# Performance work log

Measured on AMD Instinct MI355X. Metric: run time of the kernel, lower is better.

Reference implementation:

```python
import jax, jax.numpy as jnp
import numpy as np
from jax import lax

B, T, Tq, S, G, Hd, GW, V = 128, 512, 32, 64, 300, 256, 512, 159
Z = 7 * Hd + 2


def _gru_cell(x, h, Wih, Whh, bih, bhh):
    # torch.nn.GRUCell math (gate order r,z,n)
    gi = x @ Wih.T + bih
    gh = h @ Whh.T + bhh
    i_r, i_z, i_n = jnp.split(gi, 3, axis=-1)
    h_r, h_z, h_n = jnp.split(gh, 3, axis=-1)
    r = jax.nn.sigmoid(i_r + h_r)
    z = jax.nn.sigmoid(i_z + h_z)
    n = jnp.tanh(i_n + r * h_n)
    return (1.0 - z) * n + z * h


def _run_gru(x, Wih, Whh, bih, bhh):
    b = x.shape[0]
    h0 = jnp.zeros((b, Whh.shape[1]), x.dtype)
    def step(h, xt):
        h2 = _gru_cell(xt, h, Wih, Whh, bih, bhh)
        return h2, h2
    _, ys = lax.scan(step, h0, jnp.swapaxes(x, 0, 1))
    return jnp.swapaxes(ys, 0, 1)  # [B,T,H]


def _attention(C, Qv, Mv, zW, gW1, gb1, gW2, gb2):
    # Attention(C, Q, Mt_1) -> Attention_G(c, m=Q, q=Mt_1); vectorized over sentences.
    qb = Qv[:, None, :]   # question, 2nd arg 'm' in Attention_Z
    mb = Mv[:, None, :]   # memory,   3rd arg 'q' in Attention_Z
    cW = jnp.einsum('bsh,kh->bsk', C, zW)  # att_zW(c), no bias
    z = jnp.concatenate([
        C,
        jnp.broadcast_to(qb, C.shape),
        jnp.broadcast_to(mb, C.shape),
        C * mb,                       # c * q  (q = memory)
        C * qb,                       # c * m  (m = question)
        jnp.abs(C - mb),              # |c - q|
        jnp.abs(C - qb),              # |c - m|
        jnp.sum(cW * mb, -1, keepdims=True),  # diag(cW q^T)
        jnp.sum(cW * qb, -1, keepdims=True),  # diag(cW m^T)
    ], axis=-1)  # [B,S,7H+2]
    H1 = jnp.tanh(jnp.einsum('bsz,gz->bsg', z, gW1) + gb1)
    g = jax.nn.sigmoid(jnp.einsum('bsg,og->bso', H1, gW2) + gb2)
    return g[..., 0]  # [B,S]


def setup_inputs() -> dict:
    key = jax.random.key(0)
    ks = jax.random.split(key, 32)
    def p(k, shape):
        return jax.random.normal(k, shape, jnp.float32) * 0.05
    inp = {
        'input': jax.random.normal(ks[0], (B, T, G), jnp.float32),
        'Q': jax.random.normal(ks[1], (B, Tq, G), jnp.float32),
        'EOS_idx': jnp.sort(jax.random.randint(ks[2], (B, S), 0, T), axis=1),
        'q_seq_len': jax.random.randint(ks[3], (B,), 0, Tq),
        'm_depth': 3,
        'a_len': 1,
        # GRU_i
        'Wih_i': p(ks[4], (3 * Hd, G)), 'Whh_i': p(ks[5], (3 * Hd, Hd)),
        'bih_i': p(ks[6], (3 * Hd,)), 'bhh_i': p(ks[7], (3 * Hd,)),
        # GRU_q
        'Wih_q': p(ks[8], (3 * Hd, G)), 'Whh_q': p(ks[9], (3 * Hd, Hd)),
        'bih_q': p(ks[10], (3 * Hd,)), 'bhh_q': p(ks[11], (3 * Hd,)),
        # attention
        'zW': p(ks[12], (Hd, Hd)),
        'gW1': p(ks[13], (GW, Z)), 'gb1': p(ks[14], (GW,)),
        'gW2': p(ks[15], (1, GW)), 'gb2': p(ks[16], (1,)),
        # GRUcell_m
        'Wih_m': p(ks[17], (3 * Hd, Hd)), 'Whh_m': p(ks[18], (3 * Hd, Hd)),
        'bih_m': p(ks[19], (3 * Hd,)), 'bhh_m': p(ks[20], (3 * Hd,)),
        # answer module
        'Wa': p(ks[21], (V, Hd)),
        'Wih_a': p(ks[22], (3 * Hd, Hd + V)), 'Whh_a': p(ks[23], (3 * Hd, Hd)),
        'bih_a': p(ks[24], (3 * Hd,)), 'bhh_a': p(ks[25], (3 * Hd,)),
    }
    return inp


def reference(input, Q, EOS_idx, q_seq_len, m_depth, a_len,
              Wih_i, Whh_i, bih_i, bhh_i,
              Wih_q, Whh_q, bih_q, bhh_q,
              zW, gW1, gb1, gW2, gb2,
              Wih_m, Whh_m, bih_m, bhh_m,
              Wa, Wih_a, Whh_a, bih_a, bhh_a):
    b = input.shape[0]
    # InputModule2: GRU over words, gather hidden states at EOS positions -> facts
    out_i = _run_gru(input, Wih_i, Whh_i, bih_i, bhh_i)          # [B,T,H]
    facts = out_i[jnp.arange(b)[:, None], EOS_idx]               # [B,S,H]
    # QuestionModule2: last valid hidden state of question GRU
    out_q = _run_gru(Q, Wih_q, Whh_q, bih_q, bhh_q)              # [B,Tq,H]
    qidx = jnp.clip(q_seq_len - 1, 0, Q.shape[1] - 1)
    q = out_q[jnp.arange(b), qidx]                               # [B,H]
    # MemoryUpdate (mode='softmax')
    Mt = q
    atts = []
    for _ in range(m_depth):
        att = _attention(facts, q, Mt, zW, gW1, gb1, gW2, gb2)   # [B,S]
        atts.append(att[:, None, :])
        soft = jax.nn.softmax(att, axis=1)
        Htc = jnp.einsum('bsh,bs->bh', facts, soft)              # SoftmaxRep
        Mt = _gru_cell(Htc, Mt, Wih_m, Whh_m, bih_m, bhh_m)
    Attentions = jnp.concatenate(atts, axis=1)                   # [B,depth,S]
    # AnswerModule
    at = Mt
    yt = jax.nn.softmax(at @ Wa.T, axis=1)
    preds = []
    for _ in range(a_len):
        xt = jnp.concatenate([yt, q], axis=1)
        at = _gru_cell(xt, at, Wih_a, Whh_a, bih_a, bhh_a)
        yt = jax.nn.softmax(at @ Wa.T, axis=1)
        preds.append(yt)
    pred = jnp.concatenate(preds, axis=1)                        # [B, a_len*159]
    return pred
```

## Files before the change

kernel.cpp:

```cpp
#include <hip/hip_runtime.h>
#include <hip/hip_bf16.h>

#define B_   128
#define T_   512
#define TQ_  32
#define S_   64
#define G_   300
#define GP_  320
#define HD_  256
#define GW_  512
#define V_   159
#define Z_   1794
#define ZP_  1824
#define H3_  768

using bf16x8 = __attribute__((ext_vector_type(8))) short;
using bf16x4 = __attribute__((ext_vector_type(4))) short;
using f32x4  = __attribute__((ext_vector_type(4))) float;

#define OFF_WIHB_I 0u
#define OFF_WIHB_Q 491520u
#define OFF_GW1B   983040u
#define OFF_FACTS  2850816u
#define OFF_QVEC   11239424u
#define OFF_UQ     11370496u
#define OFF_UM     11501568u
#define OFF_MT     11632640u
#define OFF_B2I    13139968u
#define OFF_B2Q    13143040u
#define OFF_QBF    13500416u
#define OFF_ABF    16777216u
#define OFF_GIQ    20971520u
#define OFF_Z      29360128u
#define OFF_WMXT   59768832u
#define OFF_WMHT   60555264u
#define OFF_WAXT   61341696u
#define OFF_WAHT   62616576u
#define OFF_GII    67108864u
#define OFF_H1     67108864u

#define WAIT_LGKM0() __builtin_amdgcn_s_waitcnt(0xC07F)

__device__ __forceinline__ unsigned short f2bf(float f) {
    unsigned int u = __float_as_uint(f);
    u += 0x7fffu + ((u >> 16) & 1u);
    return (unsigned short)(u >> 16);
}
__device__ __forceinline__ float bf2f(unsigned short s) {
    return __uint_as_float(((unsigned int)s) << 16);
}
__device__ __forceinline__ float rcpf(float x) { return __builtin_amdgcn_rcpf(x); }
__device__ __forceinline__ float sigm(float x) { return rcpf(1.f + __expf(-x)); }
__device__ __forceinline__ float tanh_fast(float x) {
    float e = __expf(-2.f * fabsf(x));
    float t = (1.f - e) * rcpf(1.f + e);
    return copysignf(t, x);
}

#define S1_ 196608
#define S2_ 318720
#define S3_ 768
#define S4_ 245760
#define S5_ 933888
#define S6_ 1310720
#define S7_ 20971520
#define PREP_TOT (S1_ + S2_ + S3_ + S4_ + S5_ + S6_ + S7_)
__global__ void prep_kernel(
    const float* __restrict__ Wih_m, float* __restrict__ WmxT,
    const float* __restrict__ Whh_m, float* __restrict__ WmhT,
    const float* __restrict__ Wih_a, float* __restrict__ WaxT,
    const float* __restrict__ Whh_a, float* __restrict__ WahT,
    const float* __restrict__ bih_i, const float* __restrict__ bhh_i, float* __restrict__ b2i,
    const float* __restrict__ bih_q, const float* __restrict__ bhh_q, float* __restrict__ b2q,
    const float* __restrict__ Wih_i, unsigned short* __restrict__ Wihb_i,
    const float* __restrict__ Wih_q, unsigned short* __restrict__ Wihb_q,
    const float* __restrict__ gW1,   unsigned short* __restrict__ gW1b,
    const float* __restrict__ Qin,   unsigned short* __restrict__ Qbf,
    const float* __restrict__ input, unsigned short* __restrict__ Abf)
{
    int i = blockIdx.x * 256 + threadIdx.x;
    if (i < S1_) {
        int r = i / 256, k = i - r * 256;
        WmxT[(size_t)k * 768 + r] = Wih_m[i];
        WmhT[(size_t)k * 768 + r] = Whh_m[i];
        WahT[(size_t)k * 768 + r] = Whh_a[i];
        return;
    }
    i -= S1_;
    if (i < S2_) {
        int r = i / 415, k = i - r * 415;
        WaxT[(size_t)k * 768 + r] = Wih_a[i];
        return;
    }
    i -= S2_;
    if (i < S3_) {
        b2i[i] = bih_i[i] + (i < 512 ? bhh_i[i] : 0.f);
        b2q[i] = bih_q[i] + (i < 512 ? bhh_q[i] : 0.f);
        return;
    }
    i -= S3_;
    if (i < S4_) {
        int r = i / GP_, c = i - r * GP_;
        Wihb_i[i] = (c < G_) ? f2bf(Wih_i[(size_t)r * G_ + c]) : (unsigned short)0;
        Wihb_q[i] = (c < G_) ? f2bf(Wih_q[(size_t)r * G_ + c]) : (unsigned short)0;
        return;
    }
    i -= S4_;
    if (i < S5_) {
        int r = i / ZP_, c = i - r * ZP_;
        gW1b[i] = (c < Z_) ? f2bf(gW1[(size_t)r * Z_ + c]) : (unsigned short)0;
        return;
    }
    i -= S5_;
    if (i < S6_) {
        int r = i / GP_, c = i - r * GP_;
        Qbf[i] = (c < G_) ? f2bf(Qin[(size_t)r * G_ + c]) : (unsigned short)0;
        return;
    }
    i -= S6_;
    if (i < S7_) {
        int r = i / GP_, c = i - r * GP_;
        Abf[i] = (c < G_) ? f2bf(input[(size_t)r * G_ + c]) : (unsigned short)0;
    }
}

__global__ __launch_bounds__(256) void gemm_bf16_kernel(
    const unsigned short* __restrict__ A, const unsigned short* __restrict__ W,
    const float* __restrict__ bias, void* __restrict__ Cout,
    int M, int N, int Kp, int act, int out_bf16, int mode, int logT)
{
    __shared__ unsigned short As[64][40];
    __shared__ unsigned short Bs[64][40];
    int tid  = threadIdx.x;
    int wv   = tid >> 6, lane = tid & 63;
    int l15  = lane & 15, q = lane >> 4;
    int n0   = blockIdx.x * 64, m0 = blockIdx.y * 64;
    int r    = tid >> 2, p4 = tid & 3;

    const f32x4 zero4 = {0.f, 0.f, 0.f, 0.f};
    f32x4 acc[4] = {zero4, zero4, zero4, zero4};

    for (int k0 = 0; k0 < Kp; k0 += 32) {
        *(int4*)&As[r][p4 * 8] = *(const int4*)&A[(size_t)(m0 + r) * Kp + k0 + p4 * 8];
        *(int4*)&Bs[r][p4 * 8] = *(const int4*)&W[(size_t)(n0 + r) * Kp + k0 + p4 * 8];
        __syncthreads();
        bf16x8 af = *(const bf16x8*)&As[16 * wv + l15][q * 8];
#pragma unroll
        for (int nt = 0; nt < 4; nt++) {
            bf16x8 bf = *(const bf16x8*)&Bs[16 * nt + l15][q * 8];
            acc[nt] = __builtin_amdgcn_mfma_f32_16x16x32_bf16(af, bf, acc[nt], 0, 0, 0);
        }
        __syncthreads();
    }
    int rb = q * 4;
#pragma unroll
    for (int nt = 0; nt < 4; nt++) {
        int cgate = n0 + 16 * nt + l15;
        float bv = bias ? bias[cgate] : 0.f;
#pragma unroll
        for (int i = 0; i < 4; i++) {
            int row = m0 + 16 * wv + rb + i;
            float v = acc[nt][i] + bv;
            if (act == 1) v = tanh_fast(v);
            if (mode == 1) {
                int Tl = 1 << logT;
                int b = row >> logT, t = row & (Tl - 1);
                int cc = b >> 4, l = b & 15;
                int type = cgate >> 8, h = cgate & 255;
                int wvd = h >> 5, off = h & 31;
                int ttd = off >> 4, qd = (off >> 2) & 3, id = off & 3;
                int tidd = wvd * 64 + qd * 16 + l;
                size_t addr = ((size_t)(cc * Tl + t) * 512 + tidd) * 24 + type * 8 + ttd * 4 + id;
                ((unsigned short*)Cout)[addr] = f2bf(v);
            } else if (out_bf16) {
                ((unsigned short*)Cout)[(size_t)row * N + cgate] = f2bf(v);
            } else {
                ((float*)Cout)[(size_t)row * N + cgate] = v;
            }
        }
    }
}

__global__ __launch_bounds__(512, 2) void gru_rec_kernel(
    const float* __restrict__ Whh0, const float* __restrict__ bhh0,
    const unsigned short* __restrict__ gi0, int T0, const int* __restrict__ g0, int GL0,
    float* __restrict__ dst0,
    const float* __restrict__ Whh1, const float* __restrict__ bhh1,
    const unsigned short* __restrict__ gi1, int T1, const int* __restrict__ g1, int GL1,
    float* __restrict__ dst1)
{
    __shared__ unsigned short hfr[2][8][4][16][8];
    __shared__ int glist[16 * 64];
    __shared__ int gptr[16], gr0s[2][16], gr1s[2][16];
    extern __shared__ unsigned short wnL[];

    int cb  = blockIdx.x;
    int tid = threadIdx.x;
    int wv  = tid >> 6, lane = tid & 63;
    int l15 = lane & 15, q = lane >> 4;

    const float* Whh; const float* bhh; const unsigned short* gi;
    const int* gidx; float* gdst; int T, GL, isq, c;
    if (cb < 8) { Whh = Whh0; bhh = bhh0; gi = gi0; T = T0; gidx = g0; GL = GL0; isq = 0; gdst = dst0; c = cb; }
    else        { Whh = Whh1; bhh = bhh1; gi = gi1; T = T1; gidx = g1; GL = GL1; isq = 1; gdst = dst1; c = cb - 8; }

    bf16x8 wf[5][8];
#pragma unroll
    for (int mt = 0; mt < 5; mt++) {
        int type = (mt < 4) ? (mt >> 1) : 2;
        int tt   = (mt < 4) ? (mt & 1) : 0;
        int g = type * 256 + 32 * wv + 16 * tt + l15;
#pragma unroll
        for (int ks = 0; ks < 8; ks++) {
            float4 w0 = *(const float4*)&Whh[(size_t)g * 256 + ks * 32 + q * 8];
            float4 w1 = *(const float4*)&Whh[(size_t)g * 256 + ks * 32 + q * 8 + 4];
            bf16x8 v;
            v[0] = (short)f2bf(w0.x); v[1] = (short)f2bf(w0.y);
            v[2] = (short)f2bf(w0.z); v[3] = (short)f2bf(w0.w);
            v[4] = (short)f2bf(w1.x); v[5] = (short)f2bf(w1.y);
            v[6] = (short)f2bf(w1.z); v[7] = (short)f2bf(w1.w);
            wf[mt][ks] = v;
        }
    }
    {
        int g = 512 + 32 * wv + 16 + l15;
#pragma unroll
        for (int ks = 0; ks < 8; ks++) {
            float4 w0 = *(const float4*)&Whh[(size_t)g * 256 + ks * 32 + q * 8];
            float4 w1 = *(const float4*)&Whh[(size_t)g * 256 + ks * 32 + q * 8 + 4];
            bf16x8 v;
            v[0] = (short)f2bf(w0.x); v[1] = (short)f2bf(w0.y);
            v[2] = (short)f2bf(w0.z); v[3] = (short)f2bf(w0.w);
            v[4] = (short)f2bf(w1.x); v[5] = (short)f2bf(w1.y);
            v[6] = (short)f2bf(w1.z); v[7] = (short)f2bf(w1.w);
            *(bf16x8*)&wnL[((wv * 8 + ks) * 64 + lane) * 8] = v;
        }
    }
    float bn[2][4];
#pragma unroll
    for (int tt = 0; tt < 2; tt++)
#pragma unroll
        for (int i = 0; i < 4; i++)
            bn[tt][i] = bhh[512 + 32 * wv + 16 * tt + 4 * q + i];

    for (int i2 = tid; i2 < 2048; i2 += 512) ((int*)hfr)[i2] = 0;
    for (int i2 = tid; i2 < 16 * GL; i2 += 512) {
        int b = i2 / GL, s = i2 - b * GL;
        int raw = gidx[(c * 16 + b) * GL + s];
        if (isq) { raw -= 1; if (raw < 0) raw = 0; if (raw > T - 1) raw = T - 1; }
        glist[b * 64 + s] = raw;
    }
    __syncthreads();
    if (tid < 16) {
        int p = 0;
        while (p < GL && glist[tid * 64 + p] == 0) p++;
        gr0s[0][tid] = 0; gr1s[0][tid] = p; gptr[tid] = p;
    }
    __syncthreads();

    float hprev[2][4] = {{0.f, 0.f, 0.f, 0.f}, {0.f, 0.f, 0.f, 0.f}};
    const unsigned short* gib = gi + (size_t)c * T * 12288;
    bf16x8 xa, xb, xc;
    {
        const unsigned short* pv = gib + (size_t)tid * 24;
        xa = *(const bf16x8*)pv;
        xb = *(const bf16x8*)(pv + 8);
        xc = *(const bf16x8*)(pv + 16);
    }

    const f32x4 zero4 = {0.f, 0.f, 0.f, 0.f};
    for (int t = 0; t < T; t++) {
        int cur = t & 1, nxt = cur ^ 1;
        if (tid < 16) {
            int tt1 = t + 1;
            int p = gptr[tid], pp = p;
            while (p < GL && glist[tid * 64 + p] == tt1) p++;
            gr0s[nxt][tid] = pp; gr1s[nxt][tid] = p; gptr[tid] = p;
        }
        f32x4 acc[6];
        acc[0] = zero4; acc[1] = zero4; acc[2] = zero4; acc[3] = zero4;
        {
            f32x4 b4 = {bn[0][0], bn[0][1], bn[0][2], bn[0][3]}; acc[4] = b4;
            f32x4 b5 = {bn[1][0], bn[1][1], bn[1][2], bn[1][3]}; acc[5] = b5;
        }
#pragma unroll
        for (int ks = 0; ks < 8; ks++) {
            bf16x8 hb = *(const bf16x8*)&hfr[cur][ks][q][l15][0];
            acc[0] = __builtin_amdgcn_mfma_f32_16x16x32_bf16(wf[0][ks], hb, acc[0], 0, 0, 0);
            acc[1] = __builtin_amdgcn_mfma_f32_16x16x32_bf16(wf[1][ks], hb, acc[1], 0, 0, 0);
            acc[2] = __builtin_amdgcn_mfma_f32_16x16x32_bf16(wf[2][ks], hb, acc[2], 0, 0, 0);
            acc[3] = __builtin_amdgcn_mfma_f32_16x16x32_bf16(wf[3][ks], hb, acc[3], 0, 0, 0);
            acc[4] = __builtin_amdgcn_mfma_f32_16x16x32_bf16(wf[4][ks], hb, acc[4], 0, 0, 0);
            bf16x8 w5 = *(const bf16x8*)&wnL[((wv * 8 + ks) * 64 + lane) * 8];
            acc[5] = __builtin_amdgcn_mfma_f32_16x16x32_bf16(w5, hb, acc[5], 0, 0, 0);
        }
        float h2a[2][4];
#pragma unroll
        for (int tt = 0; tt < 2; tt++) {
#pragma unroll
            for (int i = 0; i < 4; i++) {
                float r = sigm(bf2f((unsigned short)xa[tt * 4 + i]) + acc[tt][i]);
                float z = sigm(bf2f((unsigned short)xb[tt * 4 + i]) + acc[2 + tt][i]);
                float n = tanh_fast(bf2f((unsigned short)xc[tt * 4 + i]) + r * acc[4 + tt][i]);
                float h2 = (1.f - z) * n + z * hprev[tt][i];
                hprev[tt][i] = h2;
                h2a[tt][i] = h2;
            }
            bf16x4 hb;
#pragma unroll
            for (int i = 0; i < 4; i++) hb[i] = (short)f2bf(h2a[tt][i]);
            int qp = 2 * tt + (q >> 1), jb = 4 * (q & 1);
            *(bf16x4*)&hfr[nxt][wv][qp][l15][jb] = hb;
        }
        {
            int p0 = gr0s[cur][l15], p1 = gr1s[cur][l15];
            for (int s = p0; s < p1; s++) {
                float* dp = &gdst[((size_t)(c * 16 + l15) * GL + s) * 256 + 32 * wv + 4 * q];
                float4 o0 = {h2a[0][0], h2a[0][1], h2a[0][2], h2a[0][3]};
                float4 o1 = {h2a[1][0], h2a[1][1], h2a[1][2], h2a[1][3]};
                *(float4*)dp        = o0;
                *(float4*)(dp + 16) = o1;
            }
        }
        {
            int tn = (t + 1 < T) ? (t + 1) : (T - 1);
            const unsigned short* pv = gib + ((size_t)tn * 512 + tid) * 24;
            xa = *(const bf16x8*)pv;
            xb = *(const bf16x8*)(pv + 8);
            xc = *(const bf16x8*)(pv + 16);
        }
        __builtin_amdgcn_sched_barrier(0);
        WAIT_LGKM0();
        __builtin_amdgcn_s_barrier();
        __builtin_amdgcn_sched_barrier(0);
    }
}

__global__ __launch_bounds__(256) void uvec_kernel(const float* __restrict__ zW,
                                                   const float* __restrict__ v,
                                                   float* __restrict__ u_q,
                                                   float* __restrict__ u_m,
                                                   float* __restrict__ Mt) {
    int b = blockIdx.x, h = threadIdx.x;
    float a = 0.f;
    for (int k = 0; k < 256; k++) a += zW[k * 256 + h] * v[b * 256 + k];
    u_q[b * 256 + h] = a;
    u_m[b * 256 + h] = a;
    Mt[b * 256 + h]  = v[b * 256 + h];
}

__global__ __launch_bounds__(256) void build_z_kernel(
    const float* __restrict__ facts, const float* __restrict__ qv, const float* __restrict__ Mt,
    const float* __restrict__ u_m, const float* __restrict__ u_q, unsigned short* __restrict__ z)
{
    __shared__ float rm[4], rq[4], szm, szq;
    int bs = blockIdx.x;
    int b  = bs >> 6;
    int j  = threadIdx.x;
    float C  = facts[(size_t)bs * 256 + j];
    float m  = Mt[b * 256 + j];
    float qq = qv[b * 256 + j];
    float dm = C * u_m[b * 256 + j];
    float dq = C * u_q[b * 256 + j];
    for (int o = 32; o; o >>= 1) { dm += __shfl_down(dm, o); dq += __shfl_down(dq, o); }
    int wvi = j >> 6;
    if ((j & 63) == 0) { rm[wvi] = dm; rq[wvi] = dq; }
    __syncthreads();
    if (j == 0) { szm = rm[0] + rm[1] + rm[2] + rm[3]; szq = rq[0] + rq[1] + rq[2] + rq[3]; }
    __syncthreads();
    size_t zr = (size_t)bs * ZP_;
    z[zr + j]        = f2bf(C);
    z[zr + 256 + j]  = f2bf(qq);
    z[zr + 512 + j]  = f2bf(m);
    z[zr + 768 + j]  = f2bf(C * m);
    z[zr + 1024 + j] = f2bf(C * qq);
    z[zr + 1280 + j] = f2bf(fabsf(C - m));
    z[zr + 1536 + j] = f2bf(fabsf(C - qq));
    if (j == 0) { z[zr + 1792] = f2bf(szm); z[zr + 1793] = f2bf(szq); }
    if (j < ZP_ - Z_) z[zr + Z_ + j] = 0;
}

__global__ __launch_bounds__(256) void episode_tail_kernel(
    const float* __restrict__ H1, const float* __restrict__ gW2, const float* __restrict__ gb2,
    const float* __restrict__ facts,
    const float* __restrict__ WmxT, const float* __restrict__ bxm,
    const float* __restrict__ WmhT, const float* __restrict__ bhm,
    const float* __restrict__ zW,
    float* __restrict__ Mt, float* __restrict__ u_m)
{
    __shared__ float red[64][4];
    __shared__ float p64[64];
    __shared__ float xs[256];
    __shared__ float hs[256];
    __shared__ float hs2[256];
    int b = blockIdx.x, tid = threadIdx.x;
    {
        int s = tid >> 2, part = tid & 3;
        const float* h1r = H1 + ((size_t)(b * 64 + s)) * 512 + part * 128;
        const float* w2  = gW2 + part * 128;
        float a = 0.f;
        for (int k = 0; k < 128; k++) a += h1r[k] * w2[k];
        red[s][part] = a;
    }
    hs[tid] = Mt[b * 256 + tid];
    __syncthreads();
    if (tid < 64) {
        float att = sigm(red[tid][0] + red[tid][1] + red[tid][2] + red[tid][3] + gb2[0]);
        float mx = att;
        for (int o = 32; o; o >>= 1) mx = fmaxf(mx, __shfl_xor(mx, o));
        float e = __expf(att - mx);
        float sm = e;
        for (int o = 32; o; o >>= 1) sm += __shfl_xor(sm, o);
        p64[tid] = e * rcpf(sm);
    }
    __syncthreads();
    {
        float a = 0.f;
        for (int s = 0; s < 64; s++) a += facts[((size_t)b * 64 + s) * 256 + tid] * p64[s];
        xs[tid] = a;
    }
    __syncthreads();
    {
        int j = tid;
        float ar = bxm[j], az = bxm[256 + j], an = bxm[512 + j];
        for (int k = 0; k < 256; k++) {
            float xv = xs[k];
            const float* wr = &WmxT[(size_t)k * 768];
            ar += xv * wr[j]; az += xv * wr[256 + j]; an += xv * wr[512 + j];
        }
        float hr = bhm[j], hz = bhm[256 + j], hn = bhm[512 + j];
        for (int k = 0; k < 256; k++) {
            float hv = hs[k];
            const float* wr = &WmhT[(size_t)k * 768];
            hr += hv * wr[j]; hz += hv * wr[256 + j]; hn += hv * wr[512 + j];
        }
        float r = sigm(ar + hr);
        float z = sigm(az + hz);
        float n = tanh_fast(an + r * hn);
        float h2 = (1.f - z) * n + z * hs[j];
        Mt[b * 256 + j] = h2;
        hs2[j] = h2;
    }
    __syncthreads();
    {
        float a = 0.f;
        for (int k = 0; k < 256; k++) a += zW[k * 256 + tid] * hs2[k];
        u_m[b * 256 + tid] = a;
    }
}

__global__ __launch_bounds__(256) void answer_kernel(
    const float* __restrict__ Mt, const float* __restrict__ Wa, const float* __restrict__ qv,
    const float* __restrict__ WaxT, const float* __restrict__ bxa,
    const float* __restrict__ WahT, const float* __restrict__ bha,
    float* __restrict__ out)
{
    __shared__ float sc[V_];
    __shared__ float xs[416];
    __shared__ float hs[256], hs2[256];
    int b = blockIdx.x, tid = threadIdx.x;
    hs[tid] = Mt[b * 256 + tid];
    xs[V_ + tid] = qv[b * 256 + tid];
    __syncthreads();
    if (tid < V_) {
        float a = 0.f;
        for (int k = 0; k < 256; k++) a += hs[k] * Wa[(size_t)tid * 256 + k];
        sc[tid] = a;
    }
    __syncthreads();
    if (tid == 0) {
        float mx = -1e30f;
        for (int v = 0; v < V_; v++) mx = fmaxf(mx, sc[v]);
        float sm = 0.f;
        for (int v = 0; v < V_; v++) { float e = __expf(sc[v] - mx); sc[v] = e; sm += e; }
        float inv = rcpf(sm);
        for (int v = 0; v < V_; v++) sc[v] *= inv;
    }
    __syncthreads();
    if (tid < V_) xs[tid] = sc[tid];
    __syncthreads();
    {
        int j = tid;
        float ar = bxa[j], az = bxa[256 + j], an = bxa[512 + j];
        for (int k = 0; k < 415; k++) {
            float xv = xs[k];
            const float* wr = &WaxT[(size_t)k * 768];
            ar += xv * wr[j]; az += xv * wr[256 + j]; an += xv * wr[512 + j];
        }
        float hr = bha[j], hz = bha[256 + j], hn = bha[512 + j];
        for (int k = 0; k < 256; k++) {
            float hv = hs[k];
            const float* wr = &WahT[(size_t)k * 768];
            hr += hv * wr[j]; hz += hv * wr[256 + j]; hn += hv * wr[512 + j];
        }
        float r = sigm(ar + hr);
        float z = sigm(az + hz);
        float n = tanh_fast(an + r * hn);
        hs2[j] = (1.f - z) * n + z * hs[j];
    }
    __syncthreads();
    if (tid < V_) {
        float a = 0.f;
        for (int k = 0; k < 256; k++) a += hs2[k] * Wa[(size_t)tid * 256 + k];
        sc[tid] = a;
    }
    __syncthreads();
    if (tid == 0) {
        float mx = -1e30f;
        for (int v = 0; v < V_; v++) mx = fmaxf(mx, sc[v]);
        float sm = 0.f;
        for (int v = 0; v < V_; v++) { float e = __expf(sc[v] - mx); sc[v] = e; sm += e; }
        float inv = rcpf(sm);
        for (int v = 0; v < V_; v++) sc[v] *= inv;
    }
    __syncthreads();
    if (tid < V_) out[b * V_ + tid] = sc[tid];
}

extern "C" void kernel_launch(void* const* d_in, const int* in_sizes, int n_in,
                              void* d_out, int out_size, void* d_ws, size_t ws_size,
                              hipStream_t stream) {
    (void)in_sizes; (void)n_in; (void)out_size; (void)ws_size;
    const float* input = (const float*)d_in[0];
    const float* Qin   = (const float*)d_in[1];
    const int*   EOS   = (const int*)d_in[2];
    const int*   qsl   = (const int*)d_in[3];
    const float* Wih_i = (const float*)d_in[6];
    const float* Whh_i = (const float*)d_in[7];
    const float* bih_i = (const float*)d_in[8];
    const float* bhh_i = (const float*)d_in[9];
    const float* Wih_q = (const float*)d_in[10];
    const float* Whh_q = (const float*)d_in[11];
    const float* bih_q = (const float*)d_in[12];
    const float* bhh_q = (const float*)d_in[13];
    const float* zW    = (const float*)d_in[14];
    const float* gW1   = (const float*)d_in[15];
    const float* gb1   = (const float*)d_in[16];
    const float* gW2   = (const float*)d_in[17];
    const float* gb2   = (const float*)d_in[18];
    const float* Wih_m = (const float*)d_in[19];
    const float* Whh_m = (const float*)d_in[20];
    const float* bih_m = (const float*)d_in[21];
    const float* bhh_m = (const float*)d_in[22];
    const float* Wa    = (const float*)d_in[23];
    const float* Wih_a = (const float*)d_in[24];
    const float* Whh_a = (const float*)d_in[25];
    const float* bih_a = (const float*)d_in[26];
    const float* bhh_a = (const float*)d_in[27];

    char* ws = (char*)d_ws;
    unsigned short* Wihb_i = (unsigned short*)(ws + OFF_WIHB_I);
    unsigned short* Wihb_q = (unsigned short*)(ws + OFF_WIHB_Q);
    unsigned short* gW1b   = (unsigned short*)(ws + OFF_GW1B);
    float* facts = (float*)(ws + OFF_FACTS);
    float* qvec  = (float*)(ws + OFF_QVEC);
    float* u_q   = (float*)(ws + OFF_UQ);
    float* u_m   = (float*)(ws + OFF_UM);
    float* Mt    = (float*)(ws + OFF_MT);
    float* b2i   = (float*)(ws + OFF_B2I);
    float* b2q   = (float*)(ws + OFF_B2Q);
    float* WmxT  = (float*)(ws + OFF_WMXT);
    float* WmhT  = (float*)(ws + OFF_WMHT);
    float* WaxT  = (float*)(ws + OFF_WAXT);
    float* WahT  = (float*)(ws + OFF_WAHT);
    unsigned short* Abf  = (unsigned short*)(ws + OFF_ABF);
    unsigned short* Qbf  = (unsigned short*)(ws + OFF_QBF);
    unsigned short* gi_q = (unsigned short*)(ws + OFF_GIQ);
    unsigned short* zbf  = (unsigned short*)(ws + OFF_Z);
    unsigned short* gi_i = (unsigned short*)(ws + OFF_GII);
    float* H1 = (float*)(ws + OFF_H1);

    hipFuncSetAttribute((const void*)gru_rec_kernel,
                        hipFuncAttributeMaxDynamicSharedMemorySize, 65536);

    prep_kernel<<<(PREP_TOT + 255) / 256, 256, 0, stream>>>(
        Wih_m, WmxT, Whh_m, WmhT, Wih_a, WaxT, Whh_a, WahT,
        bih_i, bhh_i, b2i, bih_q, bhh_q, b2q,
        Wih_i, Wihb_i, Wih_q, Wihb_q, gW1, gW1b, Qin, Qbf, input, Abf);
    gemm_bf16_kernel<<<dim3(12, 1024), 256, 0, stream>>>(Abf, Wihb_i, b2i, gi_i, 65536, H3_, GP_, 0, 1, 1, 9);
    gemm_bf16_kernel<<<dim3(12, 64), 256, 0, stream>>>(Qbf, Wihb_q, b2q, gi_q, 4096, H3_, GP_, 0, 1, 1, 5);
    gru_rec_kernel<<<16, 512, 65536, stream>>>(Whh_i, bhh_i, gi_i, T_, EOS, S_, facts,
                                               Whh_q, bhh_q, gi_q, TQ_, qsl, 1, qvec);
    uvec_kernel<<<128, 256, 0, stream>>>(zW, qvec, u_q, u_m, Mt);
    for (int ep = 0; ep < 3; ep++) {
        build_z_kernel<<<8192, 256, 0, stream>>>(facts, qvec, Mt, u_m, u_q, zbf);
        gemm_bf16_kernel<<<dim3(8, 128), 256, 0, stream>>>(zbf, gW1b, gb1, H1, 8192, GW_, ZP_, 1, 0, 0, 0);
        episode_tail_kernel<<<128, 256, 0, stream>>>(H1, gW2, gb2, facts,
                                                     WmxT, bih_m, WmhT, bhh_m, zW, Mt, u_m);
    }
    answer_kernel<<<128, 256, 0, stream>>>(Mt, Wa, qvec, WaxT, bih_a, WahT, bhh_a, (float*)d_out);
}
```

Before: 1.732 ms.

## Fuse z-feature construction into attention GEMM A-tile loading

Drops the materialized bf16 z matrix (8192x1824) and builds the z features on the fly while loading the A tile of a new GEMM kernel, reading facts, Mt and q directly. The two diagonal dot products move into a small zsum kernel that writes per-row scalars. This removes a large global write and re-read in each of the three episodes. The cost is recomputing elementwise features from fp32 facts in every N-block, and the new GEMM is a simple single-buffered 64x64 tile that may be less tuned than the generic gemm_bf16_kernel.

```diff
diff --git a/kernel.cpp b/kernel.cpp
--- a/kernel.cpp
+++ b/kernel.cpp
@@ -31,7 +31,7 @@
 #define OFF_QBF    13500416u
 #define OFF_ABF    16777216u
 #define OFF_GIQ    20971520u
-#define OFF_Z      29360128u
+#define OFF_ZS     29360128u
 #define OFF_WMXT   59768832u
 #define OFF_WMHT   60555264u
 #define OFF_WAXT   61341696u
@@ -181,6 +181,103 @@
     }
 }
 
+__global__ __launch_bounds__(256) void zsum_kernel(
+    const float* __restrict__ facts, const float* __restrict__ u_m,
+    const float* __restrict__ u_q, float* __restrict__ zs)
+{
+    int tid = threadIdx.x;
+    int bs  = blockIdx.x * 8 + (tid >> 5);
+    int ln  = tid & 31;
+    int b   = bs >> 6;
+    const float* C  = &facts[(size_t)bs * 256];
+    const float* um = &u_m[b * 256];
+    const float* uq = &u_q[b * 256];
+    float sm = 0.f, sq = 0.f;
+    for (int k = ln; k < 256; k += 32) {
+        float c = C[k];
+        sm += c * um[k];
+        sq += c * uq[k];
+    }
+    for (int o = 16; o; o >>= 1) { sm += __shfl_down(sm, o); sq += __shfl_down(sq, o); }
+    if (ln == 0) { zs[bs * 2] = sm; zs[bs * 2 + 1] = sq; }
+}
+
+__global__ __launch_bounds__(256) void gemm_h1_kernel(
+    const float* __restrict__ facts, const float* __restrict__ qv, const float* __restrict__ Mt,
+    const float* __restrict__ zs, const unsigned short* __restrict__ W,
+    const float* __restrict__ bias, float* __restrict__ H1)
+{
+    __shared__ unsigned short As[64][40];
+    __shared__ unsigned short Bs[64][40];
+    int tid  = threadIdx.x;
+    int wv   = tid >> 6, lane = tid & 63;
+    int l15  = lane & 15, q = lane >> 4;
+    int n0   = blockIdx.x * 64, m0 = blockIdx.y * 64;
+    int r    = tid >> 2, p4 = tid & 3;
+    int b    = m0 >> 6;
+
+    const f32x4 zero4 = {0.f, 0.f, 0.f, 0.f};
+    f32x4 acc[4] = {zero4, zero4, zero4, zero4};
+
+    for (int k0 = 0; k0 < ZP_; k0 += 32) {
+        {
+            int region = k0 >> 8;
+            int c0 = (k0 & 255) + p4 * 8;
+            bf16x8 v8;
+            if (region == 7) {
+#pragma unroll
+                for (int j = 0; j < 8; j++) {
+                    int zc = c0 + j;
+                    float v = (zc == 0) ? zs[(m0 + r) * 2]
+                            : (zc == 1) ? zs[(m0 + r) * 2 + 1] : 0.f;
+                    v8[j] = (short)f2bf(v);
+                }
+            } else {
+                const float* Crow = &facts[(size_t)(m0 + r) * 256];
+#pragma unroll
+                for (int j = 0; j < 8; j++) {
+                    int c = c0 + j;
+                    float Cv = Crow[c];
+                    float mv = Mt[b * 256 + c];
+                    float qq = qv[b * 256 + c];
+                    float v;
+                    switch (region) {
+                        case 0:  v = Cv;              break;
+                        case 1:  v = qq;              break;
+                        case 2:  v = mv;              break;
+                        case 3:  v = Cv * mv;         break;
+                        case 4:  v = Cv * qq;         break;
+                        case 5:  v = fabsf(Cv - mv);  break;
+                        default: v = fabsf(Cv - qq);  break;
+                    }
+                    v8[j] = (short)f2bf(v);
+                }
+            }
+            *(bf16x8*)&As[r][p4 * 8] = v8;
+        }
+        *(int4*)&Bs[r][p4 * 8] = *(const int4*)&W[(size_t)(n0 + r) * ZP_ + k0 + p4 * 8];
+        __syncthreads();
+        bf16x8 af = *(const bf16x8*)&As[16 * wv + l15][q * 8];
+#pragma unroll
+        for (int nt = 0; nt < 4; nt++) {
+            bf16x8 bf = *(const bf16x8*)&Bs[16 * nt + l15][q * 8];
+            acc[nt] = __builtin_amdgcn_mfma_f32_16x16x32_bf16(af, bf, acc[nt], 0, 0, 0);
+        }
+        __syncthreads();
+    }
+    int rb = q * 4;
+#pragma unroll
+    for (int nt = 0; nt < 4; nt++) {
+        int cg = n0 + 16 * nt + l15;
+        float bv = bias[cg];
+#pragma unroll
+        for (int i = 0; i < 4; i++) {
+            int row = m0 + 16 * wv + rb + i;
+            H1[(size_t)row * GW_ + cg] = tanh_fast(acc[nt][i] + bv);
+        }
+    }
+}
+
 __global__ __launch_bounds__(512, 2) void gru_rec_kernel(
     const float* __restrict__ Whh0, const float* __restrict__ bhh0,
     const unsigned short* __restrict__ gi0, int T0, const int* __restrict__ g0, int GL0,
@@ -347,37 +444,6 @@
     u_q[b * 256 + h] = a;
     u_m[b * 256 + h] = a;
     Mt[b * 256 + h]  = v[b * 256 + h];
-}
-
-__global__ __launch_bounds__(256) void build_z_kernel(
-    const float* __restrict__ facts, const float* __restrict__ qv, const float* __restrict__ Mt,
-    const float* __restrict__ u_m, const float* __restrict__ u_q, unsigned short* __restrict__ z)
-{
-    __shared__ float rm[4], rq[4], szm, szq;
-    int bs = blockIdx.x;
-    int b  = bs >> 6;
-    int j  = threadIdx.x;
-    float C  = facts[(size_t)bs * 256 + j];
-    float m  = Mt[b * 256 + j];
-    float qq = qv[b * 256 + j];
-    float dm = C * u_m[b * 256 + j];
-    float dq = C * u_q[b * 256 + j];
-    for (int o = 32; o; o >>= 1) { dm += __shfl_down(dm, o); dq += __shfl_down(dq, o); }
-    int wvi = j >> 6;
-    if ((j & 63) == 0) { rm[wvi] = dm; rq[wvi] = dq; }
-    __syncthreads();
-    if (j == 0) { szm = rm[0] + rm[1] + rm[2] + rm[3]; szq = rq[0] + rq[1] + rq[2] + rq[3]; }
-    __syncthreads();
-    size_t zr = (size_t)bs * ZP_;
-    z[zr + j]        = f2bf(C);
-    z[zr + 256 + j]  = f2bf(qq);
-    z[zr + 512 + j]  = f2bf(m);
-    z[zr + 768 + j]  = f2bf(C * m);
-    z[zr + 1024 + j] = f2bf(C * qq);
-    z[zr + 1280 + j] = f2bf(fabsf(C - m));
-    z[zr + 1536 + j] = f2bf(fabsf(C - qq));
-    if (j == 0) { z[zr + 1792] = f2bf(szm); z[zr + 1793] = f2bf(szq); }
-    if (j < ZP_ - Z_) z[zr + Z_ + j] = 0;
 }
 
 __global__ __launch_bounds__(256) void episode_tail_kernel(
@@ -559,6 +625,7 @@
     float* Mt    = (float*)(ws + OFF_MT);
     float* b2i   = (float*)(ws + OFF_B2I);
     float* b2q   = (float*)(ws + OFF_B2Q);
+    float* zs    = (float*)(ws + OFF_ZS);
     float* WmxT  = (float*)(ws + OFF_WMXT);
     float* WmhT  = (float*)(ws + OFF_WMHT);
     float* WaxT  = (float*)(ws + OFF_WAXT);
@@ -566,7 +633,6 @@
     unsigned short* Abf  = (unsigned short*)(ws + OFF_ABF);
     unsigned short* Qbf  = (unsigned short*)(ws + OFF_QBF);
     unsigned short* gi_q = (unsigned short*)(ws + OFF_GIQ);
-    unsigned short* zbf  = (unsigned short*)(ws + OFF_Z);
     unsigned short* gi_i = (unsigned short*)(ws + OFF_GII);
     float* H1 = (float*)(ws + OFF_H1);
 
@@ -583,8 +649,8 @@
                                                Whh_q, bhh_q, gi_q, TQ_, qsl, 1, qvec);
     uvec_kernel<<<128, 256, 0, stream>>>(zW, qvec, u_q, u_m, Mt);
     for (int ep = 0; ep < 3; ep++) {
-        build_z_kernel<<<8192, 256, 0, stream>>>(facts, qvec, Mt, u_m, u_q, zbf);
-        gemm_bf16_kernel<<<dim3(8, 128), 256, 0, stream>>>(zbf, gW1b, gb1, H1, 8192, GW_, ZP_, 1, 0, 0, 0);
+        zsum_kernel<<<1024, 256, 0, stream>>>(facts, u_m, u_q, zs);
+        gemm_h1_kernel<<<dim3(8, 128), 256, 0, stream>>>(facts, qvec, Mt, zs, gW1b, gb1, H1);
         episode_tail_kernel<<<128, 256, 0, stream>>>(H1, gW2, gb2, facts,
                                                      WmxT, bih_m, WmhT, bhh_m, zW, Mt, u_m);
     }
```

New measurement: 2.573 ms. 48.5% more time.
